# Kernel tuning notes

Measured on AMD Instinct MI355X. Metric: run time of the kernel, lower is better.

## Reference

```python
import jax, jax.numpy as jnp
import numpy as np

DIM = 1024
NUM_HEADS = 16
HEAD_DIM = DIM // NUM_HEADS


def setup_inputs() -> dict:
    key = jax.random.key(0)
    k1, k2, k3 = jax.random.split(key, 3)
    scale = 1.0 / np.sqrt(DIM)
    x = jax.random.normal(k1, (4, 2048, DIM), dtype=jnp.float32)
    w_qkv = jax.random.normal(k2, (DIM, 3 * DIM), dtype=jnp.float32) * scale
    b_qkv = jnp.zeros((3 * DIM,), dtype=jnp.float32)
    w_out = jax.random.normal(k3, (DIM, DIM), dtype=jnp.float32) * scale
    b_out = jnp.zeros((DIM,), dtype=jnp.float32)
    return {"x": x, "w_qkv": w_qkv, "b_qkv": b_qkv, "w_out": w_out, "b_out": b_out}


def reference(x, w_qkv, b_qkv, w_out, b_out):
    B, S, D = x.shape
    H, Hd = NUM_HEADS, HEAD_DIM
    qkv = x @ w_qkv + b_qkv  # [B,S,3D]
    q, k, v = jnp.split(qkv, 3, axis=-1)
    # [B,H,S,Hd]
    q = q.reshape(B, S, H, Hd).transpose(0, 2, 1, 3)
    k = k.reshape(B, S, H, Hd).transpose(0, 2, 1, 3)
    v = v.reshape(B, S, H, Hd).transpose(0, 2, 1, 3)
    scores = jnp.einsum('bhqd,bhkd->bhqk', q, k) / np.sqrt(Hd).astype(np.float32)
    causal = jnp.triu(jnp.ones((S, S), dtype=bool), k=1)  # True above diagonal -> masked
    scores = jnp.where(causal[None, None], -jnp.inf, scores)
    scores = scores - jnp.max(scores, axis=-1, keepdims=True)
    attn = jax.nn.softmax(scores, axis=-1)
    out = jnp.einsum('bhqk,bhkd->bhqd', attn, v)  # [B,H,S,Hd]
    out = out.transpose(0, 2, 1, 3).reshape(B, S, D)
    return out @ w_out + b_out
```

## Files before the change

### kernel.cpp

```cpp
#include <hip/hip_runtime.h>

typedef unsigned short u16;
typedef unsigned int u32;
using f32x4 = __attribute__((ext_vector_type(4))) float;
using u32x4 = __attribute__((ext_vector_type(4))) u32;
typedef u32x4 __attribute__((may_alias)) u32x4a;
typedef uint2 __attribute__((may_alias)) uint2a;
using bf16x8 = __attribute__((ext_vector_type(8))) __bf16;

#define SEQ 2048

__device__ __forceinline__ u16 f2bf(float f) {
  union { float f; u32 u; } c; c.f = f;
  return (u16)((c.u + 0x7fffu + ((c.u >> 16) & 1u)) >> 16);
}
__device__ __forceinline__ float bf2f(u16 h) {
  union { u32 u; float f; } c; c.u = ((u32)h) << 16;
  return c.f;
}
__device__ __forceinline__ bf16x8 ld16(const u16* p) {
  return __builtin_bit_cast(bf16x8, *(const u32x4a*)p);
}
__device__ __forceinline__ f32x4 mfma16(bf16x8 a, bf16x8 b, f32x4 c) {
  return __builtin_amdgcn_mfma_f32_16x16x32_bf16(a, b, c, 0, 0, 0);
}
__device__ __forceinline__ void gload_lds16(const u16* g, u16* l) {
  __builtin_amdgcn_global_load_lds(
      (const __attribute__((address_space(1))) void*)g,
      (__attribute__((address_space(3))) void*)l, 16, 0, 0);
}
__device__ __forceinline__ u32 cvtpk(float lo, float hi) {
  u32 r;
  asm("v_cvt_pk_bf16_f32 %0, %1, %2" : "=v"(r) : "v"(lo), "v"(hi));
  return r;
}
__device__ __forceinline__ void plane32_swap(u32& a, u32& b) {
  asm("v_permlane32_swap_b32 %0, %1" : "+v"(a), "+v"(b));
}
__device__ __forceinline__ f32x4 vmax4(f32x4 a, f32x4 b) {
  f32x4 r;
  r[0] = fmaxf(a[0], b[0]); r[1] = fmaxf(a[1], b[1]);
  r[2] = fmaxf(a[2], b[2]); r[3] = fmaxf(a[3], b[3]);
  return r;
}

__global__ void detect_dtype(const u16* __restrict__ x, int* __restrict__ flag) {
  if (threadIdx.x == 0) {
    int cnt = 0;
    for (int i = 0; i < 32; ++i) {
      const int e = (x[2 * i] >> 7) & 0xFF;
      cnt += (e >= 100 && e <= 140) ? 1 : 0;
    }
    *flag = (cnt >= 20) ? 1 : 0;
  }
}


__global__ __launch_bounds__(256)
void cvt_x(const void* __restrict__ in, u16* __restrict__ out,
           const int* __restrict__ flag, size_t eoff4) {
  const size_t i = (size_t)blockIdx.x * 256 + threadIdx.x;
  if (*flag) {
    ((uint2*)out)[i] = ((const uint2*)in)[eoff4 + i];
  } else {
    const float4 v = ((const float4*)in)[eoff4 + i];
    uint2 ov;
    ov.x = (u32)f2bf(v.x) | ((u32)f2bf(v.y) << 16);
    ov.y = (u32)f2bf(v.z) | ((u32)f2bf(v.w) << 16);
    ((uint2*)out)[i] = ov;
  }
}

__global__ __launch_bounds__(256)
void cvt_bias(const void* __restrict__ in, float* __restrict__ out, int n,
              const int* __restrict__ flag) {
  const int i = blockIdx.x * 256 + threadIdx.x;
  if (i >= n) return;
  out[i] = (*flag) ? bf2f(((const u16*)in)[i]) : ((const float*)in)[i];
}

__global__ __launch_bounds__(256)
void transpose_w(const void* __restrict__ in, u16* __restrict__ out, int K, int N,
                 const int* __restrict__ flag) {
  __shared__ float t[64][65];
  const int tid = threadIdx.x;
  const int r = tid >> 4, c4 = tid & 15;
  const int n0 = blockIdx.x << 6, k0 = blockIdx.y << 6;
  const int fl = *flag;
#pragma unroll
  for (int i = 0; i < 4; ++i) {
    const int kk = r + i * 16;
    const size_t base = (size_t)(k0 + kk) * N + n0 + c4 * 4;
    if (fl) {
      const uint2 raw = *(const uint2*)((const u16*)in + base);
      t[kk][c4 * 4 + 0] = bf2f((u16)(raw.x & 0xFFFF));
      t[kk][c4 * 4 + 1] = bf2f((u16)(raw.x >> 16));
      t[kk][c4 * 4 + 2] = bf2f((u16)(raw.y & 0xFFFF));
      t[kk][c4 * 4 + 3] = bf2f((u16)(raw.y >> 16));
    } else {
      const float4 v = *(const float4*)((const float*)in + base);
      t[kk][c4 * 4 + 0] = v.x; t[kk][c4 * 4 + 1] = v.y;
      t[kk][c4 * 4 + 2] = v.z; t[kk][c4 * 4 + 3] = v.w;
    }
  }
  __syncthreads();
#pragma unroll
  for (int i = 0; i < 4; ++i) {
    const int nn = r + i * 16;
    uint2 ov;
    ov.x = (u32)f2bf(t[c4 * 4 + 0][nn]) | ((u32)f2bf(t[c4 * 4 + 1][nn]) << 16);
    ov.y = (u32)f2bf(t[c4 * 4 + 2][nn]) | ((u32)f2bf(t[c4 * 4 + 3][nn]) << 16);
    *(uint2*)&out[(size_t)(n0 + nn) * K + k0 + c4 * 4] = ov;
  }
}

__global__ __launch_bounds__(256)
void transpose_v(const u16* __restrict__ qkv, u16* __restrict__ vt) {
  __shared__ __align__(16) u16 t[64][72];
  const int h = blockIdx.x, s0 = blockIdx.y << 6, b = blockIdx.z;
  const int tid = threadIdx.x;
  const int r = tid >> 2, g = tid & 3;
  const u16* src = &qkv[(size_t)(b * SEQ + s0 + r) * 3072 + 2048 + h * 64 + g * 16];
  *(u32x4a*)&t[r][g * 16]     = *(const u32x4a*)src;
  *(u32x4a*)&t[r][g * 16 + 8] = *(const u32x4a*)(src + 8);
  __syncthreads();
  union { u16 s[16]; u32x4 v[2]; } u;
#pragma unroll
  for (int e = 0; e < 16; ++e) u.s[e] = t[g * 16 + e][r];
  u16* dst = &vt[(size_t)((b * 16 + h) * 64 + r) * 2048 + s0 + g * 16];
  *(u32x4a*)dst = u.v[0];
  *(u32x4a*)(dst + 8) = u.v[1];
}

template <bool BF16_OUT>
__global__ __launch_bounds__(256)
void gemm_bt(const u16* __restrict__ A, const u16* __restrict__ BT,
             const float* __restrict__ bias, void* __restrict__ Cv,
             int M, int N, int K) {
  constexpr int BK = 32;
  __shared__ __align__(16) u16 lA[128 * BK];
  __shared__ __align__(16) u16 lB[128 * BK];
  const int tid = threadIdx.x;
  const int wid = tid >> 6, lane = tid & 63;
  const int quad = lane >> 4, l16 = lane & 15;
  const int tile_m = blockIdx.y << 7, tile_n = blockIdx.x << 7;
  const int wm = (wid >> 1) << 6, wn = (wid & 1) << 6;
  const int G0 = wid * 64 + lane, G1 = G0 + 256;
  const int r0 = G0 >> 2, c0 = (G0 & 3) * 8;
  const int r1 = G1 >> 2, c1 = (G1 & 3) * 8;
  u16* const dA0 = lA + wid * 512;
  u16* const dA1 = lA + 2048 + wid * 512;
  u16* const dB0 = lB + wid * 512;
  u16* const dB1 = lB + 2048 + wid * 512;

  f32x4 acc[4][4] = {};

  for (int k0 = 0; k0 < K; k0 += BK) {
    __syncthreads();
    gload_lds16(&A [(size_t)(tile_m + r0) * K + k0 + c0], dA0);
    gload_lds16(&BT[(size_t)(tile_n + r0) * K + k0 + c0], dB0);
    gload_lds16(&A [(size_t)(tile_m + r1) * K + k0 + c1], dA1);
    gload_lds16(&BT[(size_t)(tile_n + r1) * K + k0 + c1], dB1);
    __syncthreads();
    bf16x8 af[4], bfr[4];
#pragma unroll
    for (int i = 0; i < 4; ++i) {
      af[i]  = ld16(&lA[(wm + i * 16 + l16) * BK + quad * 8]);
      bfr[i] = ld16(&lB[(wn + i * 16 + l16) * BK + quad * 8]);
    }
#pragma unroll
    for (int i = 0; i < 4; ++i)
#pragma unroll
      for (int j = 0; j < 4; ++j) acc[i][j] = mfma16(af[i], bfr[j], acc[i][j]);
  }

#pragma unroll
  for (int j = 0; j < 4; ++j) {
    const int cg = tile_n + wn + j * 16 + l16;
    const float bv = bias[cg];
#pragma unroll
    for (int i = 0; i < 4; ++i) {
      const int rg = tile_m + wm + i * 16 + quad * 4;
#pragma unroll
      for (int r = 0; r < 4; ++r) {
        const float v = acc[i][j][r] + bv;
        if constexpr (BF16_OUT)
          ((u16*)Cv)[(size_t)(rg + r) * N + cg] = f2bf(v);
        else
          ((float*)Cv)[(size_t)(rg + r) * N + cg] = v;
      }
    }
  }
}

__global__ __launch_bounds__(256, 4)
void attn_fwd(const u16* __restrict__ qkv, const u16* __restrict__ vt,
              u16* __restrict__ aout) {
  const int h = blockIdx.x, b = blockIdx.z;
  const int tid = threadIdx.x, wid = tid >> 6, lane = tid & 63;
  const int quad = lane >> 4, l16 = lane & 15;
  const int qodd = quad & 1;
  __shared__ __align__(16) u16 lK[2][4096];
  __shared__ __align__(16) u16 lV[2][4096];

  const int G0 = wid * 64 + lane, G1 = G0 + 256;
  const int r0 = G0 >> 3, c0 = ((G0 & 7) ^ (r0 & 7)) * 8;
  const int r1 = G1 >> 3, c1 = ((G1 & 7) ^ (r1 & 7)) * 8;
  const int db0 = wid * 512, db1 = 2048 + wid * 512;

  const u16* const kg = qkv + (size_t)(b * SEQ) * 3072 + 1024 + h * 64;
  const u16* const vg = vt + (size_t)((b * 16 + h) * 64) * 2048;

  const int sl0 = (quad ^ (l16 & 7)) * 8;
  const int sl1 = sl0 ^ 32;

  const f32x4 z = {0.f, 0.f, 0.f, 0.f};
  int cur = 0;

#pragma unroll 1
  for (int pass = 0; pass < 2; ++pass) {
    const int qt = pass ? (int)blockIdx.y : 31 - (int)blockIdx.y;
    const int q0 = qt * 64 + wid * 16;
    const size_t qi = (size_t)(b * SEQ + q0 + l16) * 3072 + h * 64 + quad * 8;
    const bf16x8 aq0 = ld16(&qkv[qi]);
    const bf16x8 aq1 = ld16(&qkv[qi + 32]);
    f32x4 o[4] = {z, z, z, z};
    float m_r = -1e30f, l_r = 0.f;

    {
      gload_lds16(kg + (size_t)r0 * 3072 + c0, &lK[cur][db0]);
      gload_lds16(kg + (size_t)r1 * 3072 + c1, &lK[cur][db1]);
      gload_lds16(vg + (size_t)r0 * 2048 + c0, &lV[cur][db0]);
      gload_lds16(vg + (size_t)r1 * 2048 + c1, &lV[cur][db1]);
    }
    __syncthreads();

    for (int kt = 0; kt <= qt; ++kt) {
      if (kt < qt) {
        const int kb = (kt + 1) * 64;
        gload_lds16(kg + (size_t)(kb + r0) * 3072 + c0, &lK[cur ^ 1][db0]);
        gload_lds16(kg + (size_t)(kb + r1) * 3072 + c1, &lK[cur ^ 1][db1]);
        gload_lds16(vg + (size_t)r0 * 2048 + kb + c0, &lV[cur ^ 1][db0]);
        gload_lds16(vg + (size_t)r1 * 2048 + kb + c1, &lV[cur ^ 1][db1]);
      }
      const u16* const lKc = lK[cur];
      const u16* const lVc = lV[cur];
      f32x4 s[4];
#pragma unroll
      for (int f = 0; f < 4; ++f) {
        const int rb = (f * 16 + l16) * 64;
        f32x4 a = z;
        a = mfma16(ld16(&lKc[rb + sl0]), aq0, a);
        a = mfma16(ld16(&lKc[rb + sl1]), aq1, a);
        s[f] = a * 0.180336879f;
      }
      bf16x8 vf0[4], vf1[4];
#pragma unroll
      for (int f = 0; f < 4; ++f) {
        const int rb = (f * 16 + l16) * 64;
        vf0[f] = ld16(&lVc[rb + sl0]);
        vf1[f] = ld16(&lVc[rb + sl1]);
      }
      if (kt == qt) {
#pragma unroll
        for (int f = 0; f < 4; ++f)
#pragma unroll
          for (int r = 0; r < 4; ++r)
            if (f * 16 + quad * 4 + r > wid * 16 + l16) s[f][r] = -1e30f;
      }
      const f32x4 m4 = vmax4(vmax4(s[0], s[1]), vmax4(s[2], s[3]));
      const float pmax = fmaxf(fmaxf(m4[0], m4[1]), fmaxf(m4[2], m4[3]));
      if (__any(pmax > m_r + 8.f)) {
        float mm = fmaxf(pmax, __shfl_xor(pmax, 16));
        mm = fmaxf(mm, __shfl_xor(mm, 32));
        const float mn = fmaxf(m_r, mm);
        const float al = exp2f(m_r - mn);
        l_r *= al;
#pragma unroll
        for (int f = 0; f < 4; ++f)
#pragma unroll
          for (int r = 0; r < 4; ++r) o[f][r] *= al;
        m_r = mn;
      }
#pragma unroll
      for (int f = 0; f < 4; ++f)
#pragma unroll
        for (int r = 0; r < 4; ++r) s[f][r] = exp2f(s[f][r] - m_r);
      const f32x4 s4 = (s[0] + s[1]) + (s[2] + s[3]);
      float sv = (s4[0] + s4[1]) + (s4[2] + s4[3]);
      sv += __shfl_xor(sv, 16);
      sv += __shfl_xor(sv, 32);
      l_r += sv;
      u32 u00 = cvtpk(s[0][0], s[0][1]), u01 = cvtpk(s[0][2], s[0][3]);
      u32 u10 = cvtpk(s[1][0], s[1][1]), u11 = cvtpk(s[1][2], s[1][3]);
      u32 u20 = cvtpk(s[2][0], s[2][1]), u21 = cvtpk(s[2][2], s[2][3]);
      u32 u30 = cvtpk(s[3][0], s[3][1]), u31 = cvtpk(s[3][2], s[3][3]);
      u32x4 P0, P1;
      {
        u32 A0 = u00, B0 = u10, A1 = u01, B1 = u11;
        plane32_swap(A0, B0);
        plane32_swap(A1, B1);
        u32 Y0 = qodd ? A0 : B0;
        u32 Y1 = qodd ? A1 : B1;
        Y0 = (u32)__shfl_xor((int)Y0, 16);
        Y1 = (u32)__shfl_xor((int)Y1, 16);
        P0[0] = qodd ? Y0 : A0;
        P0[1] = qodd ? Y1 : A1;
        P0[2] = qodd ? B0 : Y0;
        P0[3] = qodd ? B1 : Y1;
      }
      {
        u32 A0 = u20, B0 = u30, A1 = u21, B1 = u31;
        plane32_swap(A0, B0);
        plane32_swap(A1, B1);
        u32 Y0 = qodd ? A0 : B0;
        u32 Y1 = qodd ? A1 : B1;
        Y0 = (u32)__shfl_xor((int)Y0, 16);
        Y1 = (u32)__shfl_xor((int)Y1, 16);
        P1[0] = qodd ? Y0 : A0;
        P1[1] = qodd ? Y1 : A1;
        P1[2] = qodd ? B0 : Y0;
        P1[3] = qodd ? B1 : Y1;
      }
      const bf16x8 pb0 = __builtin_bit_cast(bf16x8, P0);
      const bf16x8 pb1 = __builtin_bit_cast(bf16x8, P1);
#pragma unroll
      for (int f = 0; f < 4; ++f) {
        o[f] = mfma16(vf0[f], pb0, o[f]);
        o[f] = mfma16(vf1[f], pb1, o[f]);
      }
      __syncthreads();
      cur ^= 1;
    }
    const float inv = 1.0f / l_r;
#pragma unroll
    for (int f = 0; f < 4; ++f) {
      uint2a wv;
      wv.x = cvtpk(o[f][0] * inv, o[f][1] * inv);
      wv.y = cvtpk(o[f][2] * inv, o[f][3] * inv);
      *(uint2a*)&aout[(size_t)(b * SEQ + q0 + l16) * 1024 + h * 64 + f * 16 +
                      quad * 4] = wv;
    }
  }
}

extern "C" void kernel_launch(void* const* d_in, const int* in_sizes, int n_in,
                              void* d_out, int out_size, void* d_ws, size_t ws_size,
                              hipStream_t stream) {
  const void* x     = d_in[0];
  const void* w_qkv = d_in[1];
  const void* b_qkv = d_in[2];
  const void* w_out = d_in[3];
  const void* b_out = d_in[4];
  float* out = (float*)d_out;

  float* bqf   = (float*)d_ws;
  float* bof   = bqf + 3072;
  int*   flag  = (int*)(bof + 1024);
  u16*   wqkvT = (u16*)(flag + 4);
  u16*   woutT = wqkvT + (size_t)3072 * 1024;
  u16*   xb    = woutT + (size_t)1024 * 1024;

  detect_dtype<<<dim3(1), dim3(64), 0, stream>>>((const u16*)x, flag);
  cvt_bias<<<dim3(12), dim3(256), 0, stream>>>(b_qkv, bqf, 3072, flag);
  cvt_bias<<<dim3(4), dim3(256), 0, stream>>>(b_out, bof, 1024, flag);
  transpose_w<<<dim3(48, 16), dim3(256), 0, stream>>>(w_qkv, wqkvT, 1024, 3072, flag);
  transpose_w<<<dim3(16, 16), dim3(256), 0, stream>>>(w_out, woutT, 1024, 1024, flag);

  const size_t FULL_WS = 92291088;
  if (ws_size >= FULL_WS) {
    u16* qkv = xb  + (size_t)8192 * 1024;
    u16* vt  = qkv + (size_t)8192 * 3072;
    cvt_x<<<dim3(8192), dim3(256), 0, stream>>>(x, xb, flag, 0);
    gemm_bt<true ><<<dim3(24, 64), dim3(256), 0, stream>>>(xb, wqkvT, bqf, qkv,
                                                           8192, 3072, 1024);
    transpose_v<<<dim3(16, 32, 4), dim3(256), 0, stream>>>(qkv, vt);
    attn_fwd<<<dim3(16, 16, 4), dim3(256), 0, stream>>>(qkv, vt, xb);
    gemm_bt<false><<<dim3(8, 64), dim3(256), 0, stream>>>(xb, woutT, bof, out,
                                                          8192, 1024, 1024);
  } else {
    u16* qkvb = xb   + (size_t)2048 * 1024;
    u16* vtb  = qkvb + (size_t)2048 * 3072;
    for (int b = 0; b < 4; ++b) {
      const size_t eoff4 = (size_t)b * 2048 * 1024 / 4;
      cvt_x<<<dim3(2048), dim3(256), 0, stream>>>(x, xb, flag, eoff4);
      gemm_bt<true ><<<dim3(24, 16), dim3(256), 0, stream>>>(xb, wqkvT, bqf, qkvb,
                                                             2048, 3072, 1024);
      transpose_v<<<dim3(16, 32, 1), dim3(256), 0, stream>>>(qkvb, vtb);
      attn_fwd<<<dim3(16, 16, 1), dim3(256), 0, stream>>>(qkvb, vtb, xb);
      gemm_bt<false><<<dim3(8, 16), dim3(256), 0, stream>>>(
          xb, woutT, bof, out + (size_t)b * 2048 * 1024, 2048, 1024, 1024);
    }
  }
}
```

Before: 333.5 us.

## Pipeline GEMM with 4-stage LDS ring, swizzle, 256x128 tiles and XCD remap

Rewrites the bf16 GEMM to use 512-thread blocks computing 256x128 tiles. A 4-deep LDS ring buffer prefetches three k-steps ahead, with one barrier per step instead of two. LDS columns are XOR-swizzled to reduce bank conflicts, block IDs are remapped across the 8 XCDs for cache locality, and s_setprio is raised around the MFMA burst. This aims to hide global-load latency and raise MFMA utilisation in the QKV and output projections, at the cost of 96KB of LDS per block and fewer blocks.

```diff
diff --git a/kernel.cpp b/kernel.cpp
--- a/kernel.cpp
+++ b/kernel.cpp
@@ -133,54 +133,87 @@
 }
 
 template <bool BF16_OUT>
-__global__ __launch_bounds__(256)
+__global__ __launch_bounds__(512, 2)
 void gemm_bt(const u16* __restrict__ A, const u16* __restrict__ BT,
              const float* __restrict__ bias, void* __restrict__ Cv,
              int M, int N, int K) {
   constexpr int BK = 32;
-  __shared__ __align__(16) u16 lA[128 * BK];
-  __shared__ __align__(16) u16 lB[128 * BK];
+  __shared__ __align__(16) u16 ring[4][12288];
   const int tid = threadIdx.x;
   const int wid = tid >> 6, lane = tid & 63;
   const int quad = lane >> 4, l16 = lane & 15;
-  const int tile_m = blockIdx.y << 7, tile_n = blockIdx.x << 7;
-  const int wm = (wid >> 1) << 6, wn = (wid & 1) << 6;
-  const int G0 = wid * 64 + lane, G1 = G0 + 256;
-  const int r0 = G0 >> 2, c0 = (G0 & 3) * 8;
-  const int r1 = G1 >> 2, c1 = (G1 & 3) * 8;
-  u16* const dA0 = lA + wid * 512;
-  u16* const dA1 = lA + 2048 + wid * 512;
-  u16* const dB0 = lB + wid * 512;
-  u16* const dB1 = lB + 2048 + wid * 512;
-
+
+  const int nbx = gridDim.x, nwg = nbx * gridDim.y;
+  int bid = blockIdx.y * nbx + blockIdx.x;
+  if ((nwg & 7) == 0) bid = (bid & 7) * (nwg >> 3) + (bid >> 3);
+  const int tile_n = (bid % nbx) << 7;
+  const int tile_m = (bid / nbx) << 8;
+
+  const int wmR = (wid >> 1) << 6;
+  const int wnR = (wid & 1) << 6;
+
+  const int G0 = wid * 64 + lane;
+  const int rA0 = G0 >> 2;
+  const int sA0 = (((G0 & 3) ^ ((rA0 & 3) ^ ((rA0 >> 2) & 3)))) * 8;
+  const int G1 = G0 + 512;
+  const int rA1 = G1 >> 2;
+  const int sA1 = (((G1 & 3) ^ ((rA1 & 3) ^ ((rA1 >> 2) & 3)))) * 8;
+  const u16* const pA0 = A + (size_t)(tile_m + rA0) * K + sA0;
+  const u16* const pA1 = A + (size_t)(tile_m + rA1) * K + sA1;
+  const u16* const pB0 = BT + (size_t)(tile_n + rA0) * K + sA0;
+  const int dst0 = wid * 512;
+  const int dst1 = 4096 + wid * 512;
+  const int dstB = 8192 + wid * 512;
+
+  const int swl = (l16 & 3) ^ ((l16 >> 2) & 3);
+  const int cA = (quad ^ swl) * 8;
+
+  const int nk = K >> 5;
   f32x4 acc[4][4] = {};
 
-  for (int k0 = 0; k0 < K; k0 += BK) {
-    __syncthreads();
-    gload_lds16(&A [(size_t)(tile_m + r0) * K + k0 + c0], dA0);
-    gload_lds16(&BT[(size_t)(tile_n + r0) * K + k0 + c0], dB0);
-    gload_lds16(&A [(size_t)(tile_m + r1) * K + k0 + c1], dA1);
-    gload_lds16(&BT[(size_t)(tile_n + r1) * K + k0 + c1], dB1);
-    __syncthreads();
+  auto STAGE = [&](int kt) {
+    u16* bp = ring[kt & 3];
+    const size_t ko = (size_t)kt * BK;
+    gload_lds16(pA0 + ko, bp + dst0);
+    gload_lds16(pA1 + ko, bp + dst1);
+    gload_lds16(pB0 + ko, bp + dstB);
+  };
+
+  STAGE(0);
+  if (nk > 1) STAGE(1);
+  if (nk > 2) STAGE(2);
+
+  for (int kt = 0; kt < nk; ++kt) {
+    asm volatile("s_waitcnt vmcnt(6)" ::: "memory");
+    __builtin_amdgcn_sched_barrier(0);
+    __builtin_amdgcn_s_barrier();
+    __builtin_amdgcn_sched_barrier(0);
+    if (kt + 3 < nk) STAGE(kt + 3);
+    const u16* bp = ring[kt & 3];
     bf16x8 af[4], bfr[4];
 #pragma unroll
+    for (int i = 0; i < 4; ++i)
+      af[i] = ld16(&bp[(wmR + i * 16 + l16) * BK + cA]);
+#pragma unroll
+    for (int j = 0; j < 4; ++j)
+      bfr[j] = ld16(&bp[8192 + (wnR + j * 16 + l16) * BK + cA]);
+    asm volatile("s_waitcnt lgkmcnt(0)" ::: "memory");
+    __builtin_amdgcn_sched_barrier(0);
+    __builtin_amdgcn_s_setprio(1);
+#pragma unroll
+    for (int i = 0; i < 4; ++i)
+#pragma unroll
+      for (int j = 0; j < 4; ++j) acc[i][j] = mfma16(af[i], bfr[j], acc[i][j]);
+    __builtin_amdgcn_s_setprio(0);
+  }
+
+#pragma unroll
+  for (int j = 0; j < 4; ++j) {
+    const int cg = tile_n + wnR + j * 16 + l16;
+    const float bv = bias[cg];
+#pragma unroll
     for (int i = 0; i < 4; ++i) {
-      af[i]  = ld16(&lA[(wm + i * 16 + l16) * BK + quad * 8]);
-      bfr[i] = ld16(&lB[(wn + i * 16 + l16) * BK + quad * 8]);
-    }
-#pragma unroll
-    for (int i = 0; i < 4; ++i)
-#pragma unroll
-      for (int j = 0; j < 4; ++j) acc[i][j] = mfma16(af[i], bfr[j], acc[i][j]);
-  }
-
-#pragma unroll
-  for (int j = 0; j < 4; ++j) {
-    const int cg = tile_n + wn + j * 16 + l16;
-    const float bv = bias[cg];
-#pragma unroll
-    for (int i = 0; i < 4; ++i) {
-      const int rg = tile_m + wm + i * 16 + quad * 4;
+      const int rg = tile_m + wmR + i * 16 + quad * 4;
 #pragma unroll
       for (int r = 0; r < 4; ++r) {
         const float v = acc[i][j][r] + bv;
@@ -372,11 +405,11 @@
     u16* qkv = xb  + (size_t)8192 * 1024;
     u16* vt  = qkv + (size_t)8192 * 3072;
     cvt_x<<<dim3(8192), dim3(256), 0, stream>>>(x, xb, flag, 0);
-    gemm_bt<true ><<<dim3(24, 64), dim3(256), 0, stream>>>(xb, wqkvT, bqf, qkv,
+    gemm_bt<true ><<<dim3(24, 32), dim3(512), 0, stream>>>(xb, wqkvT, bqf, qkv,
                                                            8192, 3072, 1024);
     transpose_v<<<dim3(16, 32, 4), dim3(256), 0, stream>>>(qkv, vt);
     attn_fwd<<<dim3(16, 16, 4), dim3(256), 0, stream>>>(qkv, vt, xb);
-    gemm_bt<false><<<dim3(8, 64), dim3(256), 0, stream>>>(xb, woutT, bof, out,
+    gemm_bt<false><<<dim3(8, 32), dim3(512), 0, stream>>>(xb, woutT, bof, out,
                                                           8192, 1024, 1024);
   } else {
     u16* qkvb = xb   + (size_t)2048 * 1024;
@@ -384,11 +417,11 @@
     for (int b = 0; b < 4; ++b) {
       const size_t eoff4 = (size_t)b * 2048 * 1024 / 4;
       cvt_x<<<dim3(2048), dim3(256), 0, stream>>>(x, xb, flag, eoff4);
-      gemm_bt<true ><<<dim3(24, 16), dim3(256), 0, stream>>>(xb, wqkvT, bqf, qkvb,
-                                                             2048, 3072, 1024);
+      gemm_bt<true ><<<dim3(24, 8), dim3(512), 0, stream>>>(xb, wqkvT, bqf, qkvb,
+                                                            2048, 3072, 1024);
       transpose_v<<<dim3(16, 32, 1), dim3(256), 0, stream>>>(qkvb, vtb);
       attn_fwd<<<dim3(16, 16, 1), dim3(256), 0, stream>>>(qkvb, vtb, xb);
-      gemm_bt<false><<<dim3(8, 16), dim3(256), 0, stream>>>(
+      gemm_bt<false><<<dim3(8, 8), dim3(512), 0, stream>>>(
           xb, woutT, bof, out + (size_t)b * 2048 * 1024, 2048, 1024, 1024);
     }
   }
```

Measured after the change: 307.3 us. 1.09x faster.
